# Performance work log

Hardware: AMD Instinct MI355X
Metric: run time of the kernel (lower is better)

Reference implementation:

```python
import jax, jax.numpy as jnp
import numpy as np

B, N, EMB, H = 16, 1024, 128, 8
INNER = EMB * H  # 1024
EPS = 1e-5


def setup_inputs() -> dict:
    key = jax.random.key(0)
    k1, k2, k3 = jax.random.split(key, 3)
    inputs = jax.random.normal(k1, (B, N, EMB), dtype=jnp.float32)
    ln_gamma = jnp.ones((EMB,), dtype=jnp.float32)
    ln_beta = jnp.zeros((EMB,), dtype=jnp.float32)
    w_qkv = jax.random.normal(k2, (EMB, 3 * INNER), dtype=jnp.float32) * (EMB ** -0.5)
    w_proj = jax.random.normal(k3, (INNER, EMB), dtype=jnp.float32) * (INNER ** -0.5)
    b_proj = jnp.zeros((EMB,), dtype=jnp.float32)
    return {"inputs": inputs, "ln_gamma": ln_gamma, "ln_beta": ln_beta,
            "w_qkv": w_qkv, "w_proj": w_proj, "b_proj": b_proj}


def reference(inputs, ln_gamma, ln_beta, w_qkv, w_proj, b_proj):
    scale = INNER ** -0.5
    # LayerNorm over last dim
    mu = jnp.mean(inputs, axis=-1, keepdims=True)
    var = jnp.var(inputs, axis=-1, keepdims=True)
    x = (inputs - mu) * jax.lax.rsqrt(var + EPS) * ln_gamma + ln_beta
    # QKV projection (no bias)
    qkv = x @ w_qkv                                  # [b, n, 3*inner]
    q, k, v = jnp.split(qkv, 3, axis=-1)             # each [b, n, inner]
    def to_heads(a):
        return a.reshape(B, N, H, EMB).transpose(0, 2, 1, 3)  # [b, h, n, d]
    q, k, v = to_heads(q), to_heads(k), to_heads(v)
    attn = jnp.einsum('bhid,bhjd->bhij', q * scale, k)
    attn = jax.nn.softmax(attn, axis=-1)
    out = jnp.einsum('bhij,bhjd->bhid', attn, v)     # [b, h, n, d]
    out = out.transpose(0, 2, 1, 3).reshape(B, N, INNER)
    return out @ w_proj + b_proj                     # [b, n, emb]
```

## Files before the change

kernel.cpp:

```cpp
#include <hip/hip_runtime.h>
#include <hip/hip_bf16.h>


typedef __attribute__((ext_vector_type(8))) short bf16x8;
typedef __attribute__((ext_vector_type(4))) float f32x4;

__device__ __forceinline__ unsigned short f2bf(float f) {
  unsigned int u = __float_as_uint(f);
  u += 0x7FFF + ((u >> 16) & 1);
  return (unsigned short)(u >> 16);
}

__device__ __forceinline__ void gll16(const void* g, void* l) {
  __builtin_amdgcn_global_load_lds((const __attribute__((address_space(1))) unsigned int*)g,
                                   (__attribute__((address_space(3))) unsigned int*)l, 16, 0, 0);
}

__global__ __launch_bounds__(256) void k_prep(const float* __restrict__ x,
                                              const float* __restrict__ gamma,
                                              const float* __restrict__ beta,
                                              const float* __restrict__ wqkv,
                                              const float* __restrict__ wproj,
                                              unsigned short* __restrict__ xb,
                                              unsigned short* __restrict__ wqkvT,
                                              unsigned short* __restrict__ wprojT) {
  __shared__ unsigned short T[17152];
  const int bid = blockIdx.x, tid = threadIdx.x;
  if (bid < 4096) {
    int row  = bid * 4 + (tid >> 6);
    int lane = tid & 63;
    float2 v = *reinterpret_cast<const float2*>(x + row * 128 + lane * 2);
    float s = v.x + v.y, ss = v.x * v.x + v.y * v.y;
#pragma unroll
    for (int m = 1; m < 64; m <<= 1) { s += __shfl_xor(s, m); ss += __shfl_xor(ss, m); }
    float mu   = s * (1.0f / 128.0f);
    float var  = ss * (1.0f / 128.0f) - mu * mu;
    float rstd = rsqrtf(var + 1e-5f);
    float2 g  = *reinterpret_cast<const float2*>(gamma + lane * 2);
    float2 be = *reinterpret_cast<const float2*>(beta + lane * 2);
    ushort2 o;
    o.x = f2bf((v.x - mu) * rstd * g.x + be.x);
    o.y = f2bf((v.y - mu) * rstd * g.y + be.y);
    *reinterpret_cast<ushort2*>(xb + row * 128 + lane * 2) = o;
  } else if (bid < 4144) {
    const int n0 = (bid - 4096) * 64;
#pragma unroll
    for (int i = 0; i < 32; i++) {
      int idx = i * 256 + tid;
      int k = idx >> 6, c = idx & 63;
      T[k * 70 + c] = f2bf(wqkv[k * 3072 + n0 + c]);
    }
    __syncthreads();
#pragma unroll
    for (int i = 0; i < 32; i++) {
      int idx = i * 256 + tid;
      int n = idx >> 7, k = idx & 127;
      wqkvT[(n0 + n) * 128 + k] = T[k * 70 + n];
    }
  } else {
    const int k0 = (bid - 4144) * 128;
#pragma unroll
    for (int i = 0; i < 64; i++) {
      int idx = i * 256 + tid;
      int r = idx >> 7, c = idx & 127;
      T[r * 134 + c] = f2bf(wproj[(k0 + r) * 128 + c]);
    }
    __syncthreads();
#pragma unroll
    for (int i = 0; i < 64; i++) {
      int idx = i * 256 + tid;
      int c = idx >> 7, r = idx & 127;
      wprojT[c * 1024 + k0 + r] = T[r * 134 + c];
    }
  }
}

__global__ __launch_bounds__(256) void k_qkv(const unsigned short* __restrict__ xb,
                                             const unsigned short* __restrict__ wt,
                                             unsigned short* __restrict__ qb,
                                             unsigned short* __restrict__ kb,
                                             unsigned short* __restrict__ vtb) {
  __shared__ __align__(16) unsigned short SH[32768];
  unsigned short* Xs = SH;
  unsigned short* Ws = SH + 16384;
  const int m0 = blockIdx.x * 128;
  const int n0 = blockIdx.y * 128;
  const int tid = threadIdx.x, wave = tid >> 6, lane = tid & 63;
  const int lm = lane & 15, lg = lane >> 4;
  const int wr = wave >> 1, wc = wave & 1;

#pragma unroll
  for (int ii = 0; ii < 8; ii++) {
    int row = wave * 32 + ii * 4 + (lane >> 4);
    int c = (lane & 15) ^ (row & 7);
    gll16(xb + (m0 + row) * 128 + c * 8, Xs + (wave * 32 + ii * 4) * 128);
    gll16(wt + (n0 + row) * 128 + c * 8, Ws + (wave * 32 + ii * 4) * 128);
  }
  __syncthreads();

  f32x4 acc[4][4];
#pragma unroll
  for (int i = 0; i < 4; i++)
#pragma unroll
    for (int j = 0; j < 4; j++) acc[i][j] = {0.f, 0.f, 0.f, 0.f};

#pragma unroll
  for (int k32 = 0; k32 < 4; k32++) {
    bf16x8 af[4], bfr[4];
#pragma unroll
    for (int mi = 0; mi < 4; mi++) {
      int row = wr * 64 + mi * 16 + lm;
      af[mi] = *(const bf16x8*)((const char*)(Xs + row * 128) + ((k32 * 64 + lg * 16) ^ ((lm & 7) << 4)));
    }
#pragma unroll
    for (int ni = 0; ni < 4; ni++) {
      int row = wc * 64 + ni * 16 + lm;
      bfr[ni] = *(const bf16x8*)((const char*)(Ws + row * 128) + ((k32 * 64 + lg * 16) ^ ((lm & 7) << 4)));
    }
#pragma unroll
    for (int mi = 0; mi < 4; mi++)
#pragma unroll
      for (int ni = 0; ni < 4; ni++)
        acc[mi][ni] = __builtin_amdgcn_mfma_f32_16x16x32_bf16(af[mi], bfr[ni], acc[mi][ni], 0, 0, 0);
  }

  __syncthreads();
  unsigned short* T = SH;
  const int isV = (n0 >= 2048);
  const float qscale = (n0 < 1024) ? 0.04508422f : 1.0f;
#pragma unroll
  for (int mi = 0; mi < 4; mi++)
#pragma unroll
    for (int ni = 0; ni < 4; ni++)
#pragma unroll
      for (int j = 0; j < 4; j++) {
        int mloc = wr * 64 + mi * 16 + 4 * lg + j;
        int nloc = wc * 64 + ni * 16 + lm;
        unsigned short v = f2bf(acc[mi][ni][j] * qscale);
        if (isV) T[nloc * 136 + mloc] = v;
        else     T[mloc * 136 + nloc] = v;
      }
  __syncthreads();
  const int bb = m0 >> 10, seq0 = m0 & 1023;
  const int hh = (n0 & 1023) >> 7;
  const int bh = bb * 8 + hh;
  unsigned short* outp; int rstride;
  if (n0 < 1024)      { outp = qb + (bh * 1024 + seq0) * 128; rstride = 128; }
  else if (n0 < 2048) { outp = kb + (bh * 1024 + seq0) * 128; rstride = 128; }
  else                { outp = vtb + bh * 131072 + seq0;      rstride = 1024; }
#pragma unroll
  for (int i = 0; i < 32; i++) {
    int flat = i * 512 + tid * 2;
    int row = flat >> 7, c = flat & 127;
    ushort2 v2 = *(ushort2*)&T[row * 136 + c];
    *(ushort2*)(outp + row * rstride + c) = v2;
  }
}

__global__ __launch_bounds__(256, 3) void k_flash(const unsigned short* __restrict__ qb,
                                                  const unsigned short* __restrict__ kb,
                                                  const unsigned short* __restrict__ vtb,
                                                  unsigned short* __restrict__ ob) {
  __shared__ __align__(16) unsigned short Ks[2][32][128];
  __shared__ __align__(16) unsigned short Vts[2][128][32];
  __shared__ __align__(16) unsigned short Ps[4][32][32];
  const int bi = blockIdx.x;
  const int xcd = bi & 7, g = bi >> 3;
  const int bh = xcd + 8 * (g >> 3);
  const int q0 = (g & 7) * 128;
  const int tid = threadIdx.x, wave = tid >> 6, lane = tid & 63;
  const int lm = lane & 15, lg = lane >> 4, lk8 = lg * 8;
  const int sw = (lm & 7) << 4;
  const int pvsw = ((lm >> 1) & 3) << 4;
  const int b = bh >> 3, h = bh & 7;

  const unsigned short* kbh = kb + bh * 131072;
  const unsigned short* vbh = vtb + bh * 131072;

  bf16x8 aq[2][4];
#pragma unroll
  for (int qs = 0; qs < 2; qs++) {
    const unsigned short* qrow = qb + (bh * 1024 + q0 + wave * 32 + qs * 16 + lm) * 128;
#pragma unroll
    for (int kc = 0; kc < 4; kc++) aq[qs][kc] = *(const bf16x8*)(qrow + kc * 32 + lk8);
  }

  f32x4 oacc[2][8];
#pragma unroll
  for (int qs = 0; qs < 2; qs++)
#pragma unroll
    for (int dt = 0; dt < 8; dt++) oacc[qs][dt] = {0.f, 0.f, 0.f, 0.f};
  float mrun[2] = {0.f, 0.f}, lrun[2] = {0.f, 0.f};

  auto stage = [&](int kt, int buf) {
#pragma unroll
    for (int ii = 0; ii < 2; ii++) {
      int krow = wave * 8 + ii * 4 + (lane >> 4);
      int c = (lane & 15) ^ (krow & 7);
      gll16(kbh + (kt * 32 + krow) * 128 + c * 8, &Ks[buf][wave * 8 + ii * 4][0]);
    }
#pragma unroll
    for (int ii = 0; ii < 2; ii++) {
      int vrow = wave * 32 + ii * 16 + (lane >> 2);
      int c = (lane & 3) ^ ((vrow >> 1) & 3);
      gll16(vbh + vrow * 1024 + kt * 32 + c * 8, &Vts[buf][wave * 32 + ii * 16][0]);
    }
  };

  stage(0, 0);
  __syncthreads();
  int cur = 0;

  for (int kt = 0; kt < 32; kt++) {
    if (kt < 31) stage(kt + 1, cur ^ 1);
    __builtin_amdgcn_sched_barrier(0);

    f32x4 sc[2][2];
    __builtin_amdgcn_s_setprio(1);
#pragma unroll
    for (int nt = 0; nt < 2; nt++) {
      f32x4 a0 = {0.f, 0.f, 0.f, 0.f}, a1 = {0.f, 0.f, 0.f, 0.f};
      const char* krowp = (const char*)&Ks[cur][nt * 16 + lm][0];
#pragma unroll
      for (int kc = 0; kc < 4; kc++) {
        bf16x8 ak = *(const bf16x8*)(krowp + ((kc * 64 + lg * 16) ^ sw));
        a0 = __builtin_amdgcn_mfma_f32_16x16x32_bf16(ak, aq[0][kc], a0, 0, 0, 0);
        a1 = __builtin_amdgcn_mfma_f32_16x16x32_bf16(ak, aq[1][kc], a1, 0, 0, 0);
      }
      sc[0][nt] = a0; sc[1][nt] = a1;
    }
    __builtin_amdgcn_s_setprio(0);

#pragma unroll
    for (int qs = 0; qs < 2; qs++) {
      float mx8 = fmaxf(fmaxf(fmaxf(sc[qs][0][0], sc[qs][0][1]), fmaxf(sc[qs][0][2], sc[qs][0][3])),
                        fmaxf(fmaxf(sc[qs][1][0], sc[qs][1][1]), fmaxf(sc[qs][1][2], sc[qs][1][3])));
      if (!__all(mx8 <= mrun[qs] + 8.f)) {
        float mx = fmaxf(mx8, __shfl_xor(mx8, 16));
        mx = fmaxf(mx, __shfl_xor(mx, 32));
        float mnew = fmaxf(mrun[qs], mx);
        float corr = __builtin_exp2f(mrun[qs] - mnew);
        mrun[qs] = mnew;
        lrun[qs] *= corr;
#pragma unroll
        for (int dt = 0; dt < 8; dt++)
#pragma unroll
          for (int j = 0; j < 4; j++) oacc[qs][dt][j] *= corr;
      }
      float ts = 0.f;
      char* psrow = (char*)&Ps[wave][qs * 16 + lm][0];
#pragma unroll
      for (int nt = 0; nt < 2; nt++) {
        float e0 = __builtin_exp2f(sc[qs][nt][0] - mrun[qs]);
        float e1 = __builtin_exp2f(sc[qs][nt][1] - mrun[qs]);
        float e2 = __builtin_exp2f(sc[qs][nt][2] - mrun[qs]);
        float e3 = __builtin_exp2f(sc[qs][nt][3] - mrun[qs]);
        ts += (e0 + e1) + (e2 + e3);
        unsigned int w0, w1;
        asm("v_cvt_pk_bf16_f32 %0, %1, %2" : "=v"(w0) : "v"(e0), "v"(e1));
        asm("v_cvt_pk_bf16_f32 %0, %1, %2" : "=v"(w1) : "v"(e2), "v"(e3));
        int p0 = (((2 * nt + (lg >> 1)) << 4) ^ pvsw) + 8 * (lg & 1);
        *(unsigned int*)(psrow + p0)     = w0;
        *(unsigned int*)(psrow + p0 + 4) = w1;
      }
      lrun[qs] += ts;
    }

    bf16x8 pb0 = *(const bf16x8*)((const char*)&Ps[wave][lm][0]      + ((lg << 4) ^ pvsw));
    bf16x8 pb1 = *(const bf16x8*)((const char*)&Ps[wave][16 + lm][0] + ((lg << 4) ^ pvsw));
    __builtin_amdgcn_s_setprio(1);
#pragma unroll
    for (int dt = 0; dt < 8; dt++) {
      bf16x8 av = *(const bf16x8*)((const char*)&Vts[cur][dt * 16 + lm][0] + ((lg << 4) ^ pvsw));
      oacc[0][dt] = __builtin_amdgcn_mfma_f32_16x16x32_bf16(av, pb0, oacc[0][dt], 0, 0, 0);
      oacc[1][dt] = __builtin_amdgcn_mfma_f32_16x16x32_bf16(av, pb1, oacc[1][dt], 0, 0, 0);
    }
    __builtin_amdgcn_s_setprio(0);

    __syncthreads();
    cur ^= 1;
  }

#pragma unroll
  for (int qs = 0; qs < 2; qs++) {
    float l = lrun[qs];
    l += __shfl_xor(l, 16);
    l += __shfl_xor(l, 32);
    float inv = 1.0f / l;
    unsigned short* orow = ob + ((b * 1024 + q0 + wave * 32 + qs * 16 + lm) * 8 + h) * 128;
#pragma unroll
    for (int dt = 0; dt < 8; dt++) {
#pragma unroll
      for (int pp = 0; pp < 2; pp++) {
        ushort2 o2;
        o2.x = f2bf(oacc[qs][dt][2 * pp]     * inv);
        o2.y = f2bf(oacc[qs][dt][2 * pp + 1] * inv);
        *(ushort2*)&orow[dt * 16 + 4 * lg + 2 * pp] = o2;
      }
    }
  }
}

__global__ __launch_bounds__(256) void k_proj(const unsigned short* __restrict__ ob,
                                              const unsigned short* __restrict__ wpt,
                                              const float* __restrict__ bproj,
                                              float* __restrict__ out) {
  __shared__ __align__(16) unsigned short Os[2][64][128];
  __shared__ __align__(16) unsigned short Ws2[2][128][128];
  const int m0 = blockIdx.x * 64;
  const int tid = threadIdx.x, wave = tid >> 6, lane = tid & 63;
  const int lm = lane & 15, lg = lane >> 4;
  const int wr = wave >> 1, wc = wave & 1;

  auto stage = [&](int kt, int buf) {
#pragma unroll
    for (int ii = 0; ii < 4; ii++) {
      int row = wave * 16 + ii * 4 + (lane >> 4);
      int c = (lane & 15) ^ (row & 7);
      gll16(ob + (m0 + row) * 1024 + kt * 128 + c * 8, &Os[buf][wave * 16 + ii * 4][0]);
    }
#pragma unroll
    for (int ii = 0; ii < 8; ii++) {
      int row = wave * 32 + ii * 4 + (lane >> 4);
      int c = (lane & 15) ^ (row & 7);
      gll16(wpt + row * 1024 + kt * 128 + c * 8, &Ws2[buf][wave * 32 + ii * 4][0]);
    }
  };

  f32x4 acc[2][4];
#pragma unroll
  for (int i = 0; i < 2; i++)
#pragma unroll
    for (int j = 0; j < 4; j++) acc[i][j] = {0.f, 0.f, 0.f, 0.f};

  stage(0, 0);
  __syncthreads();
  int cur = 0;

  for (int kt = 0; kt < 8; kt++) {
    if (kt < 7) stage(kt + 1, cur ^ 1);
    __builtin_amdgcn_sched_barrier(0);
#pragma unroll
    for (int k32 = 0; k32 < 4; k32++) {
      bf16x8 af[2], bfr[4];
#pragma unroll
      for (int mi = 0; mi < 2; mi++) {
        int row = wr * 32 + mi * 16 + lm;
        af[mi] = *(const bf16x8*)((const char*)&Os[cur][row][0] + ((k32 * 64 + lg * 16) ^ ((lm & 7) << 4)));
      }
#pragma unroll
      for (int ni = 0; ni < 4; ni++) {
        int row = wc * 64 + ni * 16 + lm;
        bfr[ni] = *(const bf16x8*)((const char*)&Ws2[cur][row][0] + ((k32 * 64 + lg * 16) ^ ((lm & 7) << 4)));
      }
#pragma unroll
      for (int mi = 0; mi < 2; mi++)
#pragma unroll
        for (int ni = 0; ni < 4; ni++)
          acc[mi][ni] = __builtin_amdgcn_mfma_f32_16x16x32_bf16(af[mi], bfr[ni], acc[mi][ni], 0, 0, 0);
    }
    __syncthreads();
    cur ^= 1;
  }

#pragma unroll
  for (int mi = 0; mi < 2; mi++)
#pragma unroll
    for (int ni = 0; ni < 4; ni++)
#pragma unroll
      for (int j = 0; j < 4; j++) {
        int m = m0 + wr * 32 + mi * 16 + 4 * (lane >> 4) + j;
        int n = wc * 64 + ni * 16 + lm;
        out[m * 128 + n] = acc[mi][ni][j] + bproj[n];
      }
}

extern "C" void kernel_launch(void* const* d_in, const int* in_sizes, int n_in,
                              void* d_out, int out_size, void* d_ws, size_t ws_size,
                              hipStream_t stream) {
  const float* x     = (const float*)d_in[0];
  const float* gamma = (const float*)d_in[1];
  const float* beta  = (const float*)d_in[2];
  const float* wqkv  = (const float*)d_in[3];
  const float* wproj = (const float*)d_in[4];
  const float* bproj = (const float*)d_in[5];
  float* out = (float*)d_out;

  unsigned short* ws = (unsigned short*)d_ws;
  unsigned short* xb     = ws;
  unsigned short* wqkvT  = xb + 2097152;
  unsigned short* wprojT = wqkvT + 393216;
  unsigned short* qbuf   = wprojT + 131072;
  unsigned short* kbuf   = qbuf + 16777216;
  unsigned short* vtbuf  = kbuf + 16777216;
  unsigned short* obuf   = vtbuf + 16777216;

  hipLaunchKernelGGL(k_prep, dim3(4152),    dim3(256), 0, stream, x, gamma, beta, wqkv, wproj, xb, wqkvT, wprojT);
  hipLaunchKernelGGL(k_qkv,  dim3(128, 24), dim3(256), 0, stream, xb, wqkvT, qbuf, kbuf, vtbuf);
  hipLaunchKernelGGL(k_flash, dim3(1024),   dim3(256), 0, stream, qbuf, kbuf, vtbuf, obuf);
  hipLaunchKernelGGL(k_proj, dim3(256),     dim3(256), 0, stream, obuf, wprojT, bproj, out);
}
```

Measured before the change: 165.8 us.

## Load weight fragments directly from global memory in QKV and projection GEMMs

Both the QKV and output-projection GEMMs stop staging the weight tile in LDS and instead read MFMA B-fragments straight from global memory, relying on cache reuse of the small weight matrix. The projection kernel also drops double buffering, halves its M tile to 32 rows and doubles the grid to 512 blocks to raise occupancy and cut LDS use. The cost is uncoalesced, latency-exposed global loads inside the MFMA loop and no overlap of the activation-tile load with compute in the projection kernel.

```diff
diff --git a/kernel.cpp b/kernel.cpp
--- a/kernel.cpp
+++ b/kernel.cpp
@@ -80,9 +80,8 @@
                                              unsigned short* __restrict__ qb,
                                              unsigned short* __restrict__ kb,
                                              unsigned short* __restrict__ vtb) {
-  __shared__ __align__(16) unsigned short SH[32768];
+  __shared__ __align__(16) unsigned short SH[17408];
   unsigned short* Xs = SH;
-  unsigned short* Ws = SH + 16384;
   const int m0 = blockIdx.x * 128;
   const int n0 = blockIdx.y * 128;
   const int tid = threadIdx.x, wave = tid >> 6, lane = tid & 63;
@@ -94,7 +93,6 @@
     int row = wave * 32 + ii * 4 + (lane >> 4);
     int c = (lane & 15) ^ (row & 7);
     gll16(xb + (m0 + row) * 128 + c * 8, Xs + (wave * 32 + ii * 4) * 128);
-    gll16(wt + (n0 + row) * 128 + c * 8, Ws + (wave * 32 + ii * 4) * 128);
   }
   __syncthreads();
 
@@ -103,6 +101,11 @@
   for (int i = 0; i < 4; i++)
 #pragma unroll
     for (int j = 0; j < 4; j++) acc[i][j] = {0.f, 0.f, 0.f, 0.f};
+
+  const unsigned short* wrow[4];
+#pragma unroll
+  for (int ni = 0; ni < 4; ni++)
+    wrow[ni] = wt + (n0 + wc * 64 + ni * 16 + lm) * 128 + lg * 8;
 
 #pragma unroll
   for (int k32 = 0; k32 < 4; k32++) {
@@ -113,10 +116,8 @@
       af[mi] = *(const bf16x8*)((const char*)(Xs + row * 128) + ((k32 * 64 + lg * 16) ^ ((lm & 7) << 4)));
     }
 #pragma unroll
-    for (int ni = 0; ni < 4; ni++) {
-      int row = wc * 64 + ni * 16 + lm;
-      bfr[ni] = *(const bf16x8*)((const char*)(Ws + row * 128) + ((k32 * 64 + lg * 16) ^ ((lm & 7) << 4)));
-    }
+    for (int ni = 0; ni < 4; ni++)
+      bfr[ni] = *(const bf16x8*)(wrow[ni] + k32 * 32);
 #pragma unroll
     for (int mi = 0; mi < 4; mi++)
 #pragma unroll
@@ -305,74 +306,51 @@
                                               const unsigned short* __restrict__ wpt,
                                               const float* __restrict__ bproj,
                                               float* __restrict__ out) {
-  __shared__ __align__(16) unsigned short Os[2][64][128];
-  __shared__ __align__(16) unsigned short Ws2[2][128][128];
-  const int m0 = blockIdx.x * 64;
+  __shared__ __align__(16) unsigned short Os[32][128];
+  const int m0 = blockIdx.x * 32;
   const int tid = threadIdx.x, wave = tid >> 6, lane = tid & 63;
   const int lm = lane & 15, lg = lane >> 4;
   const int wr = wave >> 1, wc = wave & 1;
 
-  auto stage = [&](int kt, int buf) {
-#pragma unroll
-    for (int ii = 0; ii < 4; ii++) {
-      int row = wave * 16 + ii * 4 + (lane >> 4);
+  const unsigned short* wrow[4];
+#pragma unroll
+  for (int ni = 0; ni < 4; ni++)
+    wrow[ni] = wpt + (wc * 64 + ni * 16 + lm) * 1024 + lg * 8;
+
+  f32x4 acc[4];
+#pragma unroll
+  for (int ni = 0; ni < 4; ni++) acc[ni] = {0.f, 0.f, 0.f, 0.f};
+
+  for (int kt = 0; kt < 8; kt++) {
+#pragma unroll
+    for (int ii = 0; ii < 2; ii++) {
+      int row = wave * 8 + ii * 4 + (lane >> 4);
       int c = (lane & 15) ^ (row & 7);
-      gll16(ob + (m0 + row) * 1024 + kt * 128 + c * 8, &Os[buf][wave * 16 + ii * 4][0]);
-    }
-#pragma unroll
-    for (int ii = 0; ii < 8; ii++) {
-      int row = wave * 32 + ii * 4 + (lane >> 4);
-      int c = (lane & 15) ^ (row & 7);
-      gll16(wpt + row * 1024 + kt * 128 + c * 8, &Ws2[buf][wave * 32 + ii * 4][0]);
-    }
-  };
-
-  f32x4 acc[2][4];
-#pragma unroll
-  for (int i = 0; i < 2; i++)
-#pragma unroll
-    for (int j = 0; j < 4; j++) acc[i][j] = {0.f, 0.f, 0.f, 0.f};
-
-  stage(0, 0);
-  __syncthreads();
-  int cur = 0;
-
-  for (int kt = 0; kt < 8; kt++) {
-    if (kt < 7) stage(kt + 1, cur ^ 1);
-    __builtin_amdgcn_sched_barrier(0);
+      gll16(ob + (m0 + row) * 1024 + kt * 128 + c * 8, &Os[wave * 8 + ii * 4][0]);
+    }
+    __syncthreads();
 #pragma unroll
     for (int k32 = 0; k32 < 4; k32++) {
-      bf16x8 af[2], bfr[4];
-#pragma unroll
-      for (int mi = 0; mi < 2; mi++) {
-        int row = wr * 32 + mi * 16 + lm;
-        af[mi] = *(const bf16x8*)((const char*)&Os[cur][row][0] + ((k32 * 64 + lg * 16) ^ ((lm & 7) << 4)));
-      }
-#pragma unroll
-      for (int ni = 0; ni < 4; ni++) {
-        int row = wc * 64 + ni * 16 + lm;
-        bfr[ni] = *(const bf16x8*)((const char*)&Ws2[cur][row][0] + ((k32 * 64 + lg * 16) ^ ((lm & 7) << 4)));
-      }
-#pragma unroll
-      for (int mi = 0; mi < 2; mi++)
-#pragma unroll
-        for (int ni = 0; ni < 4; ni++)
-          acc[mi][ni] = __builtin_amdgcn_mfma_f32_16x16x32_bf16(af[mi], bfr[ni], acc[mi][ni], 0, 0, 0);
-    }
-    __syncthreads();
-    cur ^= 1;
-  }
-
-#pragma unroll
-  for (int mi = 0; mi < 2; mi++)
-#pragma unroll
-    for (int ni = 0; ni < 4; ni++)
-#pragma unroll
-      for (int j = 0; j < 4; j++) {
-        int m = m0 + wr * 32 + mi * 16 + 4 * (lane >> 4) + j;
-        int n = wc * 64 + ni * 16 + lm;
-        out[m * 128 + n] = acc[mi][ni][j] + bproj[n];
-      }
+      bf16x8 af = *(const bf16x8*)((const char*)&Os[wr * 16 + lm][0] + ((k32 * 64 + lg * 16) ^ ((lm & 7) << 4)));
+      bf16x8 bfr[4];
+#pragma unroll
+      for (int ni = 0; ni < 4; ni++)
+        bfr[ni] = *(const bf16x8*)(wrow[ni] + kt * 128 + k32 * 32);
+#pragma unroll
+      for (int ni = 0; ni < 4; ni++)
+        acc[ni] = __builtin_amdgcn_mfma_f32_16x16x32_bf16(af, bfr[ni], acc[ni], 0, 0, 0);
+    }
+    __syncthreads();
+  }
+
+#pragma unroll
+  for (int ni = 0; ni < 4; ni++)
+#pragma unroll
+    for (int j = 0; j < 4; j++) {
+      int m = m0 + wr * 16 + 4 * lg + j;
+      int n = wc * 64 + ni * 16 + lm;
+      out[m * 128 + n] = acc[ni][j] + bproj[n];
+    }
 }
 
 extern "C" void kernel_launch(void* const* d_in, const int* in_sizes, int n_in,
@@ -398,5 +376,5 @@
   hipLaunchKernelGGL(k_prep, dim3(4152),    dim3(256), 0, stream, x, gamma, beta, wqkv, wproj, xb, wqkvT, wprojT);
   hipLaunchKernelGGL(k_qkv,  dim3(128, 24), dim3(256), 0, stream, xb, wqkvT, qbuf, kbuf, vtbuf);
   hipLaunchKernelGGL(k_flash, dim3(1024),   dim3(256), 0, stream, qbuf, kbuf, vtbuf, obuf);
-  hipLaunchKernelGGL(k_proj, dim3(256),     dim3(256), 0, stream, obuf, wprojT, bproj, out);
-}
+  hipLaunchKernelGGL(k_proj, dim3(512),     dim3(256), 0, stream, obuf, wprojT, bproj, out);
+}
```

Result: slower. 189.5 us (+14.3%).
